# Kernel optimization log

Measured on AMD Instinct MI355X. Metric: run time of the kernel, lower is better.

The kernel has to match this reference:

```python
import jax, jax.numpy as jnp
import numpy as np

WIDTH = 1024
N_HEADS = 16
EPS = 1e-5


def _layernorm(x, gamma, beta):
    m = jnp.mean(x, axis=-1, keepdims=True)
    v = jnp.mean((x - m) ** 2, axis=-1, keepdims=True)  # unbiased=False
    return (x - m) / jnp.sqrt(v + EPS) * gamma + beta


def setup_inputs() -> dict:
    key = jax.random.key(0)
    ks = jax.random.split(key, 8)
    d = WIDTH
    x = jax.random.normal(ks[0], (4, 1024, d), dtype=jnp.float32)
    # MHA params (torch.rand -> uniform [0,1); scale down for numerical sanity is NOT
    # done in the original, but uniform init matches torch.rand semantics)
    in_project = jax.random.uniform(ks[1], (3 * d, d), dtype=jnp.float32)
    out_project = jax.random.uniform(ks[2], (d, d), dtype=jnp.float32)
    ln1_gamma = jnp.ones((d,), jnp.float32)
    ln1_beta = jnp.zeros((d,), jnp.float32)
    ln2_gamma = jnp.ones((d,), jnp.float32)
    ln2_beta = jnp.zeros((d,), jnp.float32)
    w_up = jax.random.uniform(ks[3], (d, 2 * d), dtype=jnp.float32)
    b_up = jax.random.uniform(ks[4], (2 * d,), dtype=jnp.float32)
    w_down = jax.random.uniform(ks[5], (2 * d, d), dtype=jnp.float32)
    b_down = jax.random.uniform(ks[6], (d,), dtype=jnp.float32)
    return {"x": x, "in_project": in_project, "out_project": out_project,
            "ln1_gamma": ln1_gamma, "ln1_beta": ln1_beta,
            "w_up": w_up, "b_up": b_up, "w_down": w_down, "b_down": b_down,
            "ln2_gamma": ln2_gamma, "ln2_beta": ln2_beta}


def reference(x, in_project, out_project, ln1_gamma, ln1_beta,
              w_up, b_up, w_down, b_down, ln2_gamma, ln2_beta):
    B, S, d = x.shape
    H = N_HEADS
    dh = d // H

    # --- masked_attention(ln_1(x)), attn_mask is None ---
    h = _layernorm(x, ln1_gamma, ln1_beta)
    qkv = h @ in_project.T                       # [B,S,3d]
    qkv = qkv.reshape(B, S, 3, H, dh)            # 3H axis splits as (3, H)
    q, k, v = qkv[:, :, 0], qkv[:, :, 1], qkv[:, :, 2]   # [B,S,H,dh]
    scores = jnp.einsum('bqhd,bkhd->bhqk', q, k) / jnp.sqrt(jnp.float32(dh))
    attn = jax.nn.softmax(scores, axis=-1)       # materialized [B,H,S,S] as in original
    o = jnp.einsum('bhqk,bkhd->bqhd', attn, v).reshape(B, S, d)
    o = o @ out_project                          # note: NOT transposed in original
    x = x + o

    # --- ff(ln_2(x)) ---
    h2 = _layernorm(x, ln2_gamma, ln2_beta)
    ff = jnp.maximum(h2 @ w_up + b_up, 0.0) @ w_down + b_down
    return x + ff
```

## Files before the change

### kernel.cpp

```cpp
#include <hip/hip_runtime.h>
#include <hip/hip_bf16.h>


typedef short bf16x8 __attribute__((ext_vector_type(8)));
typedef float f32x4 __attribute__((ext_vector_type(4)));

__device__ __forceinline__ unsigned short f2bf(float f) {
  unsigned int u = __float_as_uint(f);
  unsigned int r = (u + 0x7fffu + ((u >> 16) & 1u)) >> 16;
  return (unsigned short)r;
}
__device__ __forceinline__ float bf2f(unsigned short h) {
  return __uint_as_float(((unsigned int)h) << 16);
}

__device__ __forceinline__ void gld16(const void* g, void* l) {
  __builtin_amdgcn_global_load_lds(
      (const __attribute__((address_space(1))) unsigned int*)g,
      (__attribute__((address_space(3))) unsigned int*)l, 16, 0, 0);
}


__global__ void cast_split_kernel(const float* __restrict__ in,
                                  unsigned short* __restrict__ hi,
                                  unsigned short* __restrict__ lo, int n) {
  int i = blockIdx.x * blockDim.x + threadIdx.x;
  int stride = gridDim.x * blockDim.x;
  for (; i < n; i += stride) {
    float v = in[i];
    unsigned short h = f2bf(v);
    hi[i] = h;
    lo[i] = f2bf(v - bf2f(h));
  }
}

__global__ void transpose3_kernel(const float* __restrict__ op,
                                  const float* __restrict__ wu,
                                  const float* __restrict__ wd,
                                  unsigned short* __restrict__ oT,
                                  unsigned short* __restrict__ uT,
                                  unsigned short* __restrict__ dT) {
  const float* in;
  unsigned short* out;
  int R, C;
  if (blockIdx.z == 0) { in = op; out = oT; R = 1024; C = 1024; }
  else if (blockIdx.z == 1) { in = wu; out = uT; R = 1024; C = 2048; }
  else { in = wd; out = dT; R = 2048; C = 1024; }
  int bc = blockIdx.x << 5;
  int br = blockIdx.y << 5;
  if (bc >= C || br >= R) return;
  __shared__ float t[32][33];
  int tx = threadIdx.x, ty = threadIdx.y;
#pragma unroll
  for (int i = ty; i < 32; i += 8)
    t[i][tx] = in[(size_t)(br + i) * C + bc + tx];
  __syncthreads();
#pragma unroll
  for (int i = ty; i < 32; i += 8)
    out[(size_t)(bc + i) * R + br + tx] = f2bf(t[tx][i]);
}


template <bool SPLIT>
__global__ __launch_bounds__(256) void ln_kernel(
    const float* __restrict__ x, const float* __restrict__ gamma,
    const float* __restrict__ beta, unsigned short* __restrict__ hi,
    unsigned short* __restrict__ lo) {
  int row = blockIdx.x, tid = threadIdx.x;
  float4 v = ((const float4*)x)[(size_t)row * 256 + tid];
  float s = v.x + v.y + v.z + v.w;
  float ss = v.x * v.x + v.y * v.y + v.z * v.z + v.w * v.w;
#pragma unroll
  for (int off = 32; off; off >>= 1) {
    s += __shfl_xor(s, off);
    ss += __shfl_xor(ss, off);
  }
  __shared__ float red[8];
  int wid = tid >> 6, lane = tid & 63;
  if (lane == 0) { red[wid] = s; red[4 + wid] = ss; }
  __syncthreads();
  s = red[0] + red[1] + red[2] + red[3];
  ss = red[4] + red[5] + red[6] + red[7];
  float mean = s * (1.f / 1024.f);
  float var = ss * (1.f / 1024.f) - mean * mean;
  float inv = rsqrtf(var + 1e-5f);
  float4 g = ((const float4*)gamma)[tid];
  float4 bt = ((const float4*)beta)[tid];
  float y[4];
  y[0] = (v.x - mean) * inv * g.x + bt.x;
  y[1] = (v.y - mean) * inv * g.y + bt.y;
  y[2] = (v.z - mean) * inv * g.z + bt.z;
  y[3] = (v.w - mean) * inv * g.w + bt.w;
  size_t o = (size_t)row * 1024 + tid * 4;
#pragma unroll
  for (int j = 0; j < 4; ++j) {
    unsigned short hb = f2bf(y[j]);
    hi[o + j] = hb;
    if (SPLIT) lo[o + j] = f2bf(y[j] - bf2f(hb));
  }
}


template <bool SPLIT, bool BIAS, bool RESID, bool RELU, bool OUTBF16,
          int OUTMODE>
__global__ __launch_bounds__(256) void gemm_kernel(
    const short* __restrict__ Ah, const short* __restrict__ Al,
    const short* __restrict__ Bh, const short* __restrict__ Bl,
    const float* __restrict__ bias, const float* __restrict__ resid,
    void* __restrict__ outp, int M, int N, int K,
    unsigned short* __restrict__ qh, unsigned short* __restrict__ ql,
    unsigned short* __restrict__ kh, unsigned short* __restrict__ kl,
    unsigned short* __restrict__ vtp) {
  __shared__ short As[2][128 * 32];
  __shared__ short Bs[2][128 * 32];
  __shared__ short As2[SPLIT ? 2 : 1][SPLIT ? 128 * 32 : 8];
  __shared__ short Bs2[SPLIT ? 2 : 1][SPLIT ? 128 * 32 : 8];

  const int tid = threadIdx.x;
  const int lane = tid & 63;
  const int wid = tid >> 6;
  const int wr = (wid >> 1) << 6;
  const int wc = (wid & 1) << 6;
  const int l15 = lane & 15, lh = lane >> 4;
  const int rowBase = blockIdx.y << 7;
  const int colBase = blockIdx.x << 7;

  const int sr = tid >> 2;
  const int sc = (tid & 3) << 3;
  const int soff = sr * 32 + sc;
  const short* Ag = Ah + (size_t)(rowBase + sr) * K + sc;
  const short* Bg = Bh + (size_t)(colBase + sr) * K + sc;
  const short* Ag2 = SPLIT ? Al + (size_t)(rowBase + sr) * K + sc : nullptr;
  const short* Bg2 = SPLIT ? Bl + (size_t)(colBase + sr) * K + sc : nullptr;

  f32x4 acc[4][4];
#pragma unroll
  for (int m = 0; m < 4; ++m)
#pragma unroll
    for (int n = 0; n < 4; ++n) acc[m][n] = (f32x4){0.f, 0.f, 0.f, 0.f};

  const int kT = K >> 5;
  {
    gld16(Ag, &As[0][soff]);
    gld16(Ag + (size_t)64 * K, &As[0][soff + 64 * 32]);
    gld16(Bg, &Bs[0][soff]);
    gld16(Bg + (size_t)64 * K, &Bs[0][soff + 64 * 32]);
    if constexpr (SPLIT) {
      gld16(Ag2, &As2[0][soff]);
      gld16(Ag2 + (size_t)64 * K, &As2[0][soff + 64 * 32]);
      gld16(Bg2, &Bs2[0][soff]);
      gld16(Bg2 + (size_t)64 * K, &Bs2[0][soff + 64 * 32]);
    }
  }

  for (int kt = 0; kt < kT; ++kt) {
    __syncthreads();
    const int cb = kt & 1;
    if (kt + 1 < kT) {
      const int nb = cb ^ 1;
      const int k0 = (kt + 1) << 5;
      gld16(Ag + k0, &As[nb][soff]);
      gld16(Ag + k0 + (size_t)64 * K, &As[nb][soff + 64 * 32]);
      gld16(Bg + k0, &Bs[nb][soff]);
      gld16(Bg + k0 + (size_t)64 * K, &Bs[nb][soff + 64 * 32]);
      if constexpr (SPLIT) {
        gld16(Ag2 + k0, &As2[nb][soff]);
        gld16(Ag2 + k0 + (size_t)64 * K, &As2[nb][soff + 64 * 32]);
        gld16(Bg2 + k0, &Bs2[nb][soff]);
        gld16(Bg2 + k0 + (size_t)64 * K, &Bs2[nb][soff + 64 * 32]);
      }
    }

    const short* Asb = As[cb];
    const short* Bsb = Bs[cb];
    bf16x8 af[4], bfr[4];
#pragma unroll
    for (int m = 0; m < 4; ++m)
      af[m] = *(const bf16x8*)&Asb[(wr + m * 16 + l15) * 32 + lh * 8];
#pragma unroll
    for (int n = 0; n < 4; ++n)
      bfr[n] = *(const bf16x8*)&Bsb[(wc + n * 16 + l15) * 32 + lh * 8];
    if constexpr (SPLIT) {
      const short* Asb2 = As2[cb];
      const short* Bsb2 = Bs2[cb];
      bf16x8 af2[4], bfr2[4];
#pragma unroll
      for (int m = 0; m < 4; ++m)
        af2[m] = *(const bf16x8*)&Asb2[(wr + m * 16 + l15) * 32 + lh * 8];
#pragma unroll
      for (int n = 0; n < 4; ++n)
        bfr2[n] = *(const bf16x8*)&Bsb2[(wc + n * 16 + l15) * 32 + lh * 8];
#pragma unroll
      for (int m = 0; m < 4; ++m)
#pragma unroll
        for (int n = 0; n < 4; ++n) {
          acc[m][n] = __builtin_amdgcn_mfma_f32_16x16x32_bf16(af[m], bfr[n], acc[m][n], 0, 0, 0);
          acc[m][n] = __builtin_amdgcn_mfma_f32_16x16x32_bf16(af[m], bfr2[n], acc[m][n], 0, 0, 0);
          acc[m][n] = __builtin_amdgcn_mfma_f32_16x16x32_bf16(af2[m], bfr[n], acc[m][n], 0, 0, 0);
        }
    } else {
#pragma unroll
      for (int m = 0; m < 4; ++m)
#pragma unroll
        for (int n = 0; n < 4; ++n)
          acc[m][n] = __builtin_amdgcn_mfma_f32_16x16x32_bf16(af[m], bfr[n], acc[m][n], 0, 0, 0);
    }
  }

  const int prow = rowBase + wr + lh * 4;
  const int pcol = colBase + wc + l15;
#pragma unroll
  for (int m = 0; m < 4; ++m) {
#pragma unroll
    for (int n = 0; n < 4; ++n) {
      const int c = pcol + n * 16;
      float badd = 0.f;
      if constexpr (BIAS) badd = bias[c];
#pragma unroll
      for (int i = 0; i < 4; ++i) {
        const int r = prow + m * 16 + i;
        float v = acc[m][n][i] + badd;
        if constexpr (OUTMODE == 1) {
          const int part = c >> 10;
          const int cc = c & 1023;
          const int head = cc >> 6, dim = cc & 63;
          const int b = r >> 10, s = r & 1023;
          size_t idx = (((size_t)(b * 16 + head)) * 1024 + s) * 64 + dim;
          if (part == 0) {
            float y = v * 0.125f;
            unsigned short hb = f2bf(y);
            qh[idx] = hb;
            ql[idx] = f2bf(y - bf2f(hb));
          } else {
            unsigned short hb = f2bf(v);
            kh[idx] = hb;
            kl[idx] = f2bf(v - bf2f(hb));
          }
        } else if constexpr (OUTMODE == 2) {
          const int head = c >> 6, dim = c & 63;
          const int b = r >> 10, s = r & 1023;
          vtp[(((size_t)(b * 16 + head)) * 64 + dim) * 1024 + s] = f2bf(v);
        } else {
          if constexpr (RESID) v += resid[(size_t)r * N + c];
          if constexpr (RELU) v = fmaxf(v, 0.f);
          if constexpr (OUTBF16)
            ((unsigned short*)outp)[(size_t)r * N + c] = f2bf(v);
          else
            ((float*)outp)[(size_t)r * N + c] = v;
        }
      }
    }
  }
}


__global__ __launch_bounds__(512, 2) void attn_mfma_kernel(
    const short* __restrict__ qhi, const short* __restrict__ qlo,
    const short* __restrict__ khi, const short* __restrict__ klo,
    const short* __restrict__ vt, unsigned short* __restrict__ o,
    int S, int H) {
  __shared__ short Kh[2][64 * 64];
  __shared__ short Kl[2][64 * 64];
  __shared__ short Vs[2][64 * 64];
  __shared__ short Pl[8][16 * 66];

  const int tid = threadIdx.x, lane = tid & 63, wid = tid >> 6;
  const int l15 = lane & 15, lh = lane >> 4;
  const int blk = blockIdx.x;
  const int j = blk >> 3;
  const int bh = ((blk & 7) << 3) + (j & 7);
  const int q0 = (j >> 3) << 7;
  const size_t hb = (size_t)bh * S * 64;

  const size_t qrow = hb + (size_t)(q0 + wid * 16 + l15) * 64;
  bf16x8 aqh[2], aql[2];
  aqh[0] = *(const bf16x8*)(qhi + qrow + lh * 8);
  aqh[1] = *(const bf16x8*)(qhi + qrow + 32 + lh * 8);
  aql[0] = *(const bf16x8*)(qlo + qrow + lh * 8);
  aql[1] = *(const bf16x8*)(qlo + qrow + 32 + lh * 8);

  float m_run[4], l_run[4];
  f32x4 acc_o[4];
#pragma unroll
  for (int i = 0; i < 4; ++i) { m_run[i] = -INFINITY; l_run[i] = 0.f; }
#pragma unroll
  for (int n = 0; n < 4; ++n) acc_o[n] = (f32x4){0.f, 0.f, 0.f, 0.f};

  const int r0 = tid >> 3, c0 = tid & 7;
  const int sw0 = ((c0 ^ (r0 & 7)) << 3);

  const int nT = S >> 6;
  {
    gld16(khi + hb + r0 * 64 + sw0, (char*)Kh[0] + tid * 16);
    gld16(klo + hb + r0 * 64 + sw0, (char*)Kl[0] + tid * 16);
    gld16(vt + hb + (size_t)r0 * S + sw0, (char*)Vs[0] + tid * 16);
  }

  for (int kt = 0; kt < nT; ++kt) {
    __syncthreads();
    const int cb = kt & 1;
    if (kt + 1 < nT) {
      const int nb = cb ^ 1;
      const size_t kb = hb + (size_t)(kt + 1) * 64 * 64;
      gld16(khi + kb + r0 * 64 + sw0, (char*)Kh[nb] + tid * 16);
      gld16(klo + kb + r0 * 64 + sw0, (char*)Kl[nb] + tid * 16);
      const short* vg = vt + hb + (size_t)(kt + 1) * 64;
      gld16(vg + (size_t)r0 * S + sw0, (char*)Vs[nb] + tid * 16);
    }

    const short* KhB = Kh[cb];
    const short* KlB = Kl[cb];
    const short* VsB = Vs[cb];

    f32x4 accs[4];
#pragma unroll
    for (int n = 0; n < 4; ++n) accs[n] = (f32x4){0.f, 0.f, 0.f, 0.f};
    __builtin_amdgcn_s_setprio(1);
#pragma unroll
    for (int n = 0; n < 4; ++n) {
      const int row = n * 16 + l15;
      const int sw = row & 7;
      const int ro = row * 64;
      bf16x8 bh0 = *(const bf16x8*)&KhB[ro + ((lh ^ sw) << 3)];
      bf16x8 bh1 = *(const bf16x8*)&KhB[ro + (((4 + lh) ^ sw) << 3)];
      bf16x8 bl0 = *(const bf16x8*)&KlB[ro + ((lh ^ sw) << 3)];
      bf16x8 bl1 = *(const bf16x8*)&KlB[ro + (((4 + lh) ^ sw) << 3)];
      accs[n] = __builtin_amdgcn_mfma_f32_16x16x32_bf16(aqh[0], bh0, accs[n], 0, 0, 0);
      accs[n] = __builtin_amdgcn_mfma_f32_16x16x32_bf16(aqh[1], bh1, accs[n], 0, 0, 0);
      accs[n] = __builtin_amdgcn_mfma_f32_16x16x32_bf16(aqh[0], bl0, accs[n], 0, 0, 0);
      accs[n] = __builtin_amdgcn_mfma_f32_16x16x32_bf16(aqh[1], bl1, accs[n], 0, 0, 0);
      accs[n] = __builtin_amdgcn_mfma_f32_16x16x32_bf16(aql[0], bh0, accs[n], 0, 0, 0);
      accs[n] = __builtin_amdgcn_mfma_f32_16x16x32_bf16(aql[1], bh1, accs[n], 0, 0, 0);
    }
    __builtin_amdgcn_s_setprio(0);

    float mt[4];
#pragma unroll
    for (int i = 0; i < 4; ++i) {
      mt[i] = fmaxf(fmaxf(accs[0][i], accs[1][i]), fmaxf(accs[2][i], accs[3][i]));
#pragma unroll
      for (int off = 1; off < 16; off <<= 1)
        mt[i] = fmaxf(mt[i], __shfl_xor(mt[i], off));
    }
    bool grow = (mt[0] > m_run[0] + 8.f) || (mt[1] > m_run[1] + 8.f) ||
                (mt[2] > m_run[2] + 8.f) || (mt[3] > m_run[3] + 8.f);
    if (__any(grow)) {
#pragma unroll
      for (int i = 0; i < 4; ++i) {
        float mn = fmaxf(m_run[i], mt[i]);
        float a = __expf(m_run[i] - mn);
        m_run[i] = mn;
        l_run[i] *= a;
#pragma unroll
        for (int n = 0; n < 4; ++n) acc_o[n][i] *= a;
      }
    }
    float lt[4] = {0.f, 0.f, 0.f, 0.f};
#pragma unroll
    for (int n = 0; n < 4; ++n)
#pragma unroll
      for (int i = 0; i < 4; ++i) {
        float p = __expf(accs[n][i] - m_run[i]);
        accs[n][i] = p;
        lt[i] += p;
      }
#pragma unroll
    for (int i = 0; i < 4; ++i) {
#pragma unroll
      for (int off = 1; off < 16; off <<= 1) lt[i] += __shfl_xor(lt[i], off);
      l_run[i] += lt[i];
    }

    short* pw = Pl[wid];
#pragma unroll
    for (int n = 0; n < 4; ++n)
#pragma unroll
      for (int i = 0; i < 4; ++i)
        pw[(lh * 4 + i) * 66 + n * 16 + l15] = (short)f2bf(accs[n][i]);

    bf16x8 pa0 = *(const bf16x8*)&pw[l15 * 66 + lh * 8];
    bf16x8 pa1 = *(const bf16x8*)&pw[l15 * 66 + 32 + lh * 8];
    __builtin_amdgcn_s_setprio(1);
#pragma unroll
    for (int n = 0; n < 4; ++n) {
      const int row = n * 16 + l15;
      const int sw = row & 7;
      const int ro = row * 64;
      bf16x8 bv0 = *(const bf16x8*)&VsB[ro + ((lh ^ sw) << 3)];
      bf16x8 bv1 = *(const bf16x8*)&VsB[ro + (((4 + lh) ^ sw) << 3)];
      acc_o[n] = __builtin_amdgcn_mfma_f32_16x16x32_bf16(pa0, bv0, acc_o[n], 0, 0, 0);
      acc_o[n] = __builtin_amdgcn_mfma_f32_16x16x32_bf16(pa1, bv1, acc_o[n], 0, 0, 0);
    }
    __builtin_amdgcn_s_setprio(0);
  }

  const int b = bh >> 4, h = bh & 15;
#pragma unroll
  for (int n = 0; n < 4; ++n)
#pragma unroll
    for (int i = 0; i < 4; ++i) {
      const int r = q0 + wid * 16 + lh * 4 + i;
      const int dim = n * 16 + l15;
      float v = acc_o[n][i] / l_run[i];
      o[((size_t)(b * S + r)) * 1024 + h * 64 + dim] = f2bf(v);
    }
}


extern "C" void kernel_launch(void* const* d_in, const int* in_sizes, int n_in,
                              void* d_out, int out_size, void* d_ws,
                              size_t ws_size, hipStream_t stream) {
  const float* x = (const float*)d_in[0];
  const float* in_project = (const float*)d_in[1];
  const float* out_project = (const float*)d_in[2];
  const float* ln1_g = (const float*)d_in[3];
  const float* ln1_b = (const float*)d_in[4];
  const float* w_up = (const float*)d_in[5];
  const float* b_up = (const float*)d_in[6];
  const float* w_down = (const float*)d_in[7];
  const float* b_down = (const float*)d_in[8];
  const float* ln2_g = (const float*)d_in[9];
  const float* ln2_b = (const float*)d_in[10];

  const int B = in_sizes[0] / (1024 * 1024);
  const int S = 1024, H = 16;
  const int M = B * S;

  char* ws = (char*)d_ws;
  short* h_hi = (short*)(ws + 0);
  short* h_lo = (short*)(ws + 8388608);
  float* x2 = (float*)(ws + 0);
  short* qhi = (short*)(ws + 16777216);
  short* qlo = (short*)(ws + 25165824);
  short* khi = (short*)(ws + 33554432);
  short* klo = (short*)(ws + 41943040);
  short* vt  = (short*)(ws + 50331648);
  short* o = (short*)(ws + 67108864);
  short* h2 = (short*)(ws + 75497472);
  short* u = (short*)(ws + 83886080);
  short* Wq_hi = (short*)(ws + 100663296);
  short* Wq_lo = (short*)(ws + 106954752);
  short* WoT = (short*)(ws + 113246208);
  short* WupT = (short*)(ws + 115343360);
  short* WdnT = (short*)(ws + 119537664);

  cast_split_kernel<<<2048, 256, 0, stream>>>(in_project, (unsigned short*)Wq_hi,
                                              (unsigned short*)Wq_lo, 3072 * 1024);
  transpose3_kernel<<<dim3(64, 64, 3), dim3(32, 8), 0, stream>>>(
      out_project, w_up, w_down, (unsigned short*)WoT, (unsigned short*)WupT,
      (unsigned short*)WdnT);

  ln_kernel<true><<<M, 256, 0, stream>>>(x, ln1_g, ln1_b, (unsigned short*)h_hi,
                                         (unsigned short*)h_lo);

  gemm_kernel<true, false, false, false, false, 1>
      <<<dim3(2048 / 128, M / 128), 256, 0, stream>>>(
          h_hi, h_lo, Wq_hi, Wq_lo, nullptr, nullptr, nullptr, M, 2048, 1024,
          (unsigned short*)qhi, (unsigned short*)qlo, (unsigned short*)khi,
          (unsigned short*)klo, nullptr);

  gemm_kernel<false, false, false, false, false, 2>
      <<<dim3(1024 / 128, M / 128), 256, 0, stream>>>(
          h_hi, nullptr, Wq_hi + (size_t)2048 * 1024, nullptr, nullptr, nullptr,
          nullptr, M, 1024, 1024, nullptr, nullptr, nullptr, nullptr,
          (unsigned short*)vt);

  attn_mfma_kernel<<<512, 512, 0, stream>>>(
      qhi, qlo, khi, klo, vt, (unsigned short*)o, S, H);

  gemm_kernel<false, false, true, false, false, 0>
      <<<dim3(1024 / 128, M / 128), 256, 0, stream>>>(
          o, nullptr, WoT, nullptr, nullptr, x, x2, M, 1024, 1024,
          nullptr, nullptr, nullptr, nullptr, nullptr);

  ln_kernel<false><<<M, 256, 0, stream>>>(x2, ln2_g, ln2_b,
                                          (unsigned short*)h2, nullptr);

  gemm_kernel<false, true, false, true, true, 0>
      <<<dim3(2048 / 128, M / 128), 256, 0, stream>>>(
          h2, nullptr, WupT, nullptr, b_up, nullptr, u, M, 2048, 1024,
          nullptr, nullptr, nullptr, nullptr, nullptr);

  gemm_kernel<false, true, true, false, false, 0>
      <<<dim3(1024 / 128, M / 128), 256, 0, stream>>>(
          u, nullptr, WdnT, nullptr, b_down, x2, d_out, M, 1024, 2048,
          nullptr, nullptr, nullptr, nullptr, nullptr);
}
```

Measured before the change: 275.1 us.

## Transpose QK^T MFMA so each lane owns one query row for softmax

Swaps the MFMA operand order so the score tile is computed transposed, giving each lane the scores for a single query row. Row max and sum then need only two cross-lane shuffles instead of four per row, with one scalar running max and sum per lane. P is packed as bf16 pairs into LDS with 32-bit stores, and the final normalization uses a reciprocal multiply in place of a divide. It adds shuffles to redistribute rescale factors and leans on the layout being exactly right for the transposed tile.

```diff
diff --git a/kernel.cpp b/kernel.cpp
--- a/kernel.cpp
+++ b/kernel.cpp
@@ -279,10 +279,8 @@
   aql[0] = *(const bf16x8*)(qlo + qrow + lh * 8);
   aql[1] = *(const bf16x8*)(qlo + qrow + 32 + lh * 8);
 
-  float m_run[4], l_run[4];
+  float m_run = -INFINITY, l_run = 0.f;
   f32x4 acc_o[4];
-#pragma unroll
-  for (int i = 0; i < 4; ++i) { m_run[i] = -INFINITY; l_run[i] = 0.f; }
 #pragma unroll
   for (int n = 0; n < 4; ++n) acc_o[n] = (f32x4){0.f, 0.f, 0.f, 0.f};
 
@@ -325,58 +323,53 @@
       bf16x8 bh1 = *(const bf16x8*)&KhB[ro + (((4 + lh) ^ sw) << 3)];
       bf16x8 bl0 = *(const bf16x8*)&KlB[ro + ((lh ^ sw) << 3)];
       bf16x8 bl1 = *(const bf16x8*)&KlB[ro + (((4 + lh) ^ sw) << 3)];
-      accs[n] = __builtin_amdgcn_mfma_f32_16x16x32_bf16(aqh[0], bh0, accs[n], 0, 0, 0);
-      accs[n] = __builtin_amdgcn_mfma_f32_16x16x32_bf16(aqh[1], bh1, accs[n], 0, 0, 0);
-      accs[n] = __builtin_amdgcn_mfma_f32_16x16x32_bf16(aqh[0], bl0, accs[n], 0, 0, 0);
-      accs[n] = __builtin_amdgcn_mfma_f32_16x16x32_bf16(aqh[1], bl1, accs[n], 0, 0, 0);
-      accs[n] = __builtin_amdgcn_mfma_f32_16x16x32_bf16(aql[0], bh0, accs[n], 0, 0, 0);
-      accs[n] = __builtin_amdgcn_mfma_f32_16x16x32_bf16(aql[1], bh1, accs[n], 0, 0, 0);
+      accs[n] = __builtin_amdgcn_mfma_f32_16x16x32_bf16(bh0, aqh[0], accs[n], 0, 0, 0);
+      accs[n] = __builtin_amdgcn_mfma_f32_16x16x32_bf16(bh1, aqh[1], accs[n], 0, 0, 0);
+      accs[n] = __builtin_amdgcn_mfma_f32_16x16x32_bf16(bl0, aqh[0], accs[n], 0, 0, 0);
+      accs[n] = __builtin_amdgcn_mfma_f32_16x16x32_bf16(bl1, aqh[1], accs[n], 0, 0, 0);
+      accs[n] = __builtin_amdgcn_mfma_f32_16x16x32_bf16(bh0, aql[0], accs[n], 0, 0, 0);
+      accs[n] = __builtin_amdgcn_mfma_f32_16x16x32_bf16(bh1, aql[1], accs[n], 0, 0, 0);
     }
     __builtin_amdgcn_s_setprio(0);
 
-    float mt[4];
-#pragma unroll
-    for (int i = 0; i < 4; ++i) {
-      mt[i] = fmaxf(fmaxf(accs[0][i], accs[1][i]), fmaxf(accs[2][i], accs[3][i]));
-#pragma unroll
-      for (int off = 1; off < 16; off <<= 1)
-        mt[i] = fmaxf(mt[i], __shfl_xor(mt[i], off));
-    }
-    bool grow = (mt[0] > m_run[0] + 8.f) || (mt[1] > m_run[1] + 8.f) ||
-                (mt[2] > m_run[2] + 8.f) || (mt[3] > m_run[3] + 8.f);
-    if (__any(grow)) {
-#pragma unroll
-      for (int i = 0; i < 4; ++i) {
-        float mn = fmaxf(m_run[i], mt[i]);
-        float a = __expf(m_run[i] - mn);
-        m_run[i] = mn;
-        l_run[i] *= a;
-#pragma unroll
-        for (int n = 0; n < 4; ++n) acc_o[n][i] *= a;
+    float m01 = fmaxf(fmaxf(accs[0][0], accs[0][1]), fmaxf(accs[0][2], accs[0][3]));
+    float m11 = fmaxf(fmaxf(accs[1][0], accs[1][1]), fmaxf(accs[1][2], accs[1][3]));
+    float m21 = fmaxf(fmaxf(accs[2][0], accs[2][1]), fmaxf(accs[2][2], accs[2][3]));
+    float m31 = fmaxf(fmaxf(accs[3][0], accs[3][1]), fmaxf(accs[3][2], accs[3][3]));
+    float mt = fmaxf(fmaxf(m01, m11), fmaxf(m21, m31));
+    mt = fmaxf(mt, __shfl_xor(mt, 16));
+    mt = fmaxf(mt, __shfl_xor(mt, 32));
+
+    if (__any(mt > m_run + 8.f)) {
+      float mn = fmaxf(m_run, mt);
+      float a = __expf(m_run - mn);
+      m_run = mn;
+      l_run *= a;
+      float a0 = __shfl(a, lh * 4 + 0);
+      float a1 = __shfl(a, lh * 4 + 1);
+      float a2 = __shfl(a, lh * 4 + 2);
+      float a3 = __shfl(a, lh * 4 + 3);
+#pragma unroll
+      for (int n = 0; n < 4; ++n) {
+        acc_o[n][0] *= a0; acc_o[n][1] *= a1;
+        acc_o[n][2] *= a2; acc_o[n][3] *= a3;
       }
     }
-    float lt[4] = {0.f, 0.f, 0.f, 0.f};
-#pragma unroll
-    for (int n = 0; n < 4; ++n)
-#pragma unroll
-      for (int i = 0; i < 4; ++i) {
-        float p = __expf(accs[n][i] - m_run[i]);
-        accs[n][i] = p;
-        lt[i] += p;
-      }
-#pragma unroll
-    for (int i = 0; i < 4; ++i) {
-#pragma unroll
-      for (int off = 1; off < 16; off <<= 1) lt[i] += __shfl_xor(lt[i], off);
-      l_run[i] += lt[i];
-    }
 
     short* pw = Pl[wid];
-#pragma unroll
-    for (int n = 0; n < 4; ++n)
-#pragma unroll
-      for (int i = 0; i < 4; ++i)
-        pw[(lh * 4 + i) * 66 + n * 16 + l15] = (short)f2bf(accs[n][i]);
+    unsigned int* pw32 = (unsigned int*)pw;
+#pragma unroll
+    for (int n = 0; n < 4; ++n) {
+      float p0 = __expf(accs[n][0] - m_run);
+      float p1 = __expf(accs[n][1] - m_run);
+      float p2 = __expf(accs[n][2] - m_run);
+      float p3 = __expf(accs[n][3] - m_run);
+      l_run += (p0 + p1) + (p2 + p3);
+      pw32[l15 * 33 + n * 8 + lh * 2 + 0] =
+          ((unsigned int)f2bf(p1) << 16) | f2bf(p0);
+      pw32[l15 * 33 + n * 8 + lh * 2 + 1] =
+          ((unsigned int)f2bf(p3) << 16) | f2bf(p2);
+    }
 
     bf16x8 pa0 = *(const bf16x8*)&pw[l15 * 66 + lh * 8];
     bf16x8 pa1 = *(const bf16x8*)&pw[l15 * 66 + 32 + lh * 8];
@@ -394,16 +387,25 @@
     __builtin_amdgcn_s_setprio(0);
   }
 
+  float lsum = l_run + __shfl_xor(l_run, 16);
+  lsum += __shfl_xor(lsum, 32);
+  float lrec = 1.0f / lsum;
+  float r0i = __shfl(lrec, lh * 4 + 0);
+  float r1i = __shfl(lrec, lh * 4 + 1);
+  float r2i = __shfl(lrec, lh * 4 + 2);
+  float r3i = __shfl(lrec, lh * 4 + 3);
+
   const int b = bh >> 4, h = bh & 15;
 #pragma unroll
-  for (int n = 0; n < 4; ++n)
+  for (int n = 0; n < 4; ++n) {
+    const int dim = n * 16 + l15;
+    const float rs[4] = {r0i, r1i, r2i, r3i};
 #pragma unroll
     for (int i = 0; i < 4; ++i) {
       const int r = q0 + wid * 16 + lh * 4 + i;
-      const int dim = n * 16 + l15;
-      float v = acc_o[n][i] / l_run[i];
-      o[((size_t)(b * S + r)) * 1024 + h * 64 + dim] = f2bf(v);
-    }
+      o[((size_t)(b * S + r)) * 1024 + h * 64 + dim] = f2bf(acc_o[n][i] * rs[i]);
+    }
+  }
 }
 
 
```

New measurement: 256.4 us. 1.07x faster.
